# Optimization experiments

Measured on AMD Instinct MI355X. Metric: run time of the kernel, lower is better.

Reference implementation:

```python
import jax, jax.numpy as jnp
import numpy as np

B, N, IN_F, OUT_F, H = 64, 256, 128, 128, 4
NEG_SLOPE = 0.2  # nn.LeakyReLU(dropout) -> slope 0.2


def setup_inputs() -> dict:
    key = jax.random.key(0)
    ks = jax.random.split(key, 10)
    h = jax.random.normal(ks[0], (B, N, IN_F), dtype=jnp.float32)
    projection_matrix = jax.random.normal(ks[1], (B, N, N), dtype=jnp.float32)
    similarity_matrix = jax.random.uniform(ks[2], (B, N, N), dtype=jnp.float32) * 2.0 - 1.0
    quadrant_matrix = jax.random.randint(ks[3], (B, N, N, 2), 0, 4, dtype=jnp.int32)
    # parameters (xavier-ish scaling)
    W = jax.random.normal(ks[4], (IN_F, OUT_F * H), dtype=jnp.float32) / np.sqrt(IN_F)
    a = jax.random.normal(ks[5], (H, 2 * OUT_F, 1), dtype=jnp.float32) / np.sqrt(2 * OUT_F)
    w_proj = jax.random.normal(ks[6], (OUT_F,), dtype=jnp.float32) / np.sqrt(OUT_F)
    w_sim = jax.random.normal(ks[7], (OUT_F,), dtype=jnp.float32) / np.sqrt(OUT_F)
    quadrant_bias = jax.random.normal(ks[8], (4, 4), dtype=jnp.float32) * 0.02
    W_concat = jax.random.normal(ks[9], (OUT_F * H, OUT_F), dtype=jnp.float32) / np.sqrt(OUT_F * H)
    return {"h": h, "projection_matrix": projection_matrix,
            "similarity_matrix": similarity_matrix, "quadrant_matrix": quadrant_matrix,
            "W": W, "a": a, "w_proj": w_proj, "w_sim": w_sim,
            "quadrant_bias": quadrant_bias, "W_concat": W_concat}


def reference(h, projection_matrix, similarity_matrix, quadrant_matrix,
              W, a, w_proj, w_sim, quadrant_bias, W_concat):
    b, n, _ = h.shape
    # Wh_heads: (B, H, N, F)
    Wh = (h @ W).reshape(b, n, H, OUT_F).transpose(0, 2, 1, 3)
    # GAT score: a^T [Wh_i || Wh_j] decomposes into two rank-1 terms
    a1, a2 = a[:, :OUT_F, 0], a[:, OUT_F:, 0]            # (H, F) each
    e_i = jnp.einsum('bhnf,hf->bhn', Wh, a1)
    e_j = jnp.einsum('bhnf,hf->bhn', Wh, a2)
    e = e_i[:, :, :, None] + e_j[:, :, None, :]          # (B, H, N, N)
    e = jnp.where(e > 0, e, NEG_SLOPE * e)               # leaky relu
    # projection bias: <Wh_i, proj[b,i,j] * w_proj> = (Wh_i . w_proj) * proj[b,i,j]
    s_proj = jnp.einsum('bhnf,f->bhn', Wh, w_proj)
    e = e + s_proj[:, :, :, None] * projection_matrix[:, None, :, :]
    # similarity bias, same factored form
    s_sim = jnp.einsum('bhnf,f->bhn', Wh, w_sim)
    e = e + s_sim[:, :, :, None] * similarity_matrix[:, None, :, :]
    # quadrant bias gather
    qb = quadrant_bias[quadrant_matrix[..., 0], quadrant_matrix[..., 1]]  # (B, N, N)
    e = e + qb[:, None, :, :]
    attn = jax.nn.softmax(e, axis=-1)                    # dropout is identity in eval
    h_prime = jnp.einsum('bhij,bhjf->bhif', attn, Wh)    # (B, H, N, F)
    h_prime = h_prime.transpose(0, 2, 1, 3).reshape(b, n, H * OUT_F) @ W_concat
    return jax.nn.elu(h_prime)
```

## Files before the change

### kernel.cpp

```cpp
#include <hip/hip_runtime.h>
#include <math.h>

#define BB 64
#define NN 256
#define IN_F 128
#define OF 128
#define HH 4
#define NEG_SLOPE 0.2f

typedef __attribute__((ext_vector_type(8))) short short8;
typedef __attribute__((ext_vector_type(4))) float f32x4;

#define MFMA16(a, b, c) __builtin_amdgcn_mfma_f32_16x16x32_bf16(a, b, c, 0, 0, 0)

__device__ inline unsigned short f2bf(float x) {
    unsigned u = __float_as_uint(x);
    u += 0x7fff + ((u >> 16) & 1);
    return (unsigned short)(u >> 16);
}

__global__ __launch_bounds__(256) void k0_prep(const int* __restrict__ qm,
        const float* __restrict__ W, const float* __restrict__ Wc,
        unsigned char* __restrict__ qidx, unsigned short* __restrict__ Wt,
        unsigned short* __restrict__ Wct) {
    __shared__ float hl[16][516];
    int blk = blockIdx.x, t = threadIdx.x;
    if (blk < 2048) {
        const int4* qp = (const int4*)qm;
        size_t base = (size_t)blk * 1024;
#pragma unroll
        for (int it = 0; it < 4; it++) {
            size_t i4 = base + it * 256 + t;
            int4 v = qp[i4];
            unsigned short pk = (unsigned short)((v.x * 4 + v.y) | ((v.z * 4 + v.w) << 8));
            ((unsigned short*)qidx)[i4] = pk;
        }
    } else if (blk < 2056) {
        int k0 = (blk - 2048) * 16;
#pragma unroll
        for (int it = 0; it < 8; it++) {
            int li = it * 256 + t;
            int row = li >> 7, col4 = li & 127;
            float4 v = ((const float4*)(W + (size_t)(k0 + row) * 512))[col4];
            *(float4*)&hl[row][col4 * 4] = v;
        }
        __syncthreads();
#pragma unroll
        for (int cc = 0; cc < 2; cc++) {
            int c = t * 2 + cc;
            short8 s0, s1;
#pragma unroll
            for (int k = 0; k < 8; k++) s0[k] = (short)f2bf(hl[k][c]);
#pragma unroll
            for (int k = 0; k < 8; k++) s1[k] = (short)f2bf(hl[k + 8][c]);
            unsigned short* dst = Wt + (size_t)c * 128 + k0;
            *(short8*)dst = s0;
            *(short8*)(dst + 8) = s1;
        }
    } else {
        int k0 = (blk - 2056) * 16;
#pragma unroll
        for (int it = 0; it < 2; it++) {
            int li = it * 256 + t;
            int row = li >> 5, col4 = li & 31;
            float4 v = ((const float4*)(Wc + (size_t)(k0 + row) * 128))[col4];
            *(float4*)&hl[row][col4 * 4] = v;
        }
        __syncthreads();
        if (t < 128) {
            int c = t;
            short8 s0, s1;
#pragma unroll
            for (int k = 0; k < 8; k++) s0[k] = (short)f2bf(hl[k][c]);
#pragma unroll
            for (int k = 0; k < 8; k++) s1[k] = (short)f2bf(hl[k + 8][c]);
            unsigned short* dst = Wct + (size_t)c * 512 + k0;
            *(short8*)dst = s0;
            *(short8*)(dst + 8) = s1;
        }
    }
}

__global__ __launch_bounds__(256) void k1_wh(const float* __restrict__ h,
        const unsigned short* __restrict__ Wt, const float* __restrict__ a,
        const float* __restrict__ w_proj, const float* __restrict__ w_sim,
        unsigned short* __restrict__ Wht, float* __restrict__ ei,
        float* __restrict__ ej, float* __restrict__ sp, float* __restrict__ ss) {
    __shared__ __align__(16) unsigned char hs[8192];
    __shared__ float a1s[512], a2s[512], wps[128], wss[128];
    int l = blockIdx.x;
    int b = l >> 3, n0 = (l & 7) * 32;
    int t = threadIdx.x;
    for (int idx = t; idx < 512; idx += 256) {
        int hh = idx >> 7, f = idx & 127;
        a1s[idx] = a[hh * 256 + f];
        a2s[idx] = a[hh * 256 + 128 + f];
    }
    if (t < 128) { wps[t] = w_proj[t]; wss[t] = w_sim[t]; }
    {
        const float4* hsrc = (const float4*)(h + ((size_t)b * NN + n0) * IN_F);
#pragma unroll
        for (int it = 0; it < 4; it++) {
            int li = it * 256 + t;
            float4 v = hsrc[li];
            int row = li >> 5, col4 = li & 31;
            ushort4 o;
            o.x = f2bf(v.x); o.y = f2bf(v.y); o.z = f2bf(v.z); o.w = f2bf(v.w);
            *(ushort4*)(hs + row * 256 + ((col4 * 8) ^ ((row & 7) << 4))) = o;
        }
    }
    __syncthreads();

    int w = t >> 6, lane = t & 63;
    int cc = lane & 15, g = lane >> 4;

    short8 bh[2][4];
#pragma unroll
    for (int tn = 0; tn < 2; tn++) {
        int row = tn * 16 + cc;
#pragma unroll
        for (int ks = 0; ks < 4; ks++)
            bh[tn][ks] = *(const short8*)(hs + row * 256 + ((ks * 64 + g * 16) ^ ((row & 7) << 4)));
    }

    float q[2][4][4] = {{{0.f}}};
    unsigned short* whb = Wht + (size_t)(b * HH + w) * OF * NN;

#pragma unroll
    for (int tf = 0; tf < 8; tf++) {
        int f = tf * 16 + cc;
        short8 aw[4];
#pragma unroll
        for (int ks = 0; ks < 4; ks++)
            aw[ks] = *(const short8*)(Wt + (size_t)(w * 128 + f) * IN_F + ks * 32 + g * 8);
        f32x4 acc[2];
        acc[0] = (f32x4)(0.f); acc[1] = (f32x4)(0.f);
#pragma unroll
        for (int ks = 0; ks < 4; ks++) {
            acc[0] = MFMA16(bh[0][ks], aw[ks], acc[0]);
            acc[1] = MFMA16(bh[1][ks], aw[ks], acc[1]);
        }
        float c1 = a1s[w * 128 + f], c2 = a2s[w * 128 + f];
        float c3 = wps[f], c4 = wss[f];
#pragma unroll
        for (int tn = 0; tn < 2; tn++) {
            ushort4 o;
            o.x = f2bf(acc[tn][0]); o.y = f2bf(acc[tn][1]);
            o.z = f2bf(acc[tn][2]); o.w = f2bf(acc[tn][3]);
            *(ushort4*)(whb + (size_t)f * NN + n0 + tn * 16 + g * 4) = o;
#pragma unroll
            for (int r = 0; r < 4; r++) {
                float v = acc[tn][r];
                q[tn][0][r] += v * c1; q[tn][1][r] += v * c2;
                q[tn][2][r] += v * c3; q[tn][3][r] += v * c4;
            }
        }
    }
#pragma unroll
    for (int tn = 0; tn < 2; tn++)
#pragma unroll
        for (int ty = 0; ty < 4; ty++)
#pragma unroll
            for (int r = 0; r < 4; r++) {
                float v = q[tn][ty][r];
                v += __shfl_xor(v, 1); v += __shfl_xor(v, 2);
                v += __shfl_xor(v, 4); v += __shfl_xor(v, 8);
                q[tn][ty][r] = v;
            }
    if (cc == 0) {
#pragma unroll
        for (int tn = 0; tn < 2; tn++) {
            size_t base = (size_t)(b * HH + w) * NN + n0 + tn * 16 + g * 4;
            *(float4*)&ei[base] = make_float4(q[tn][0][0], q[tn][0][1], q[tn][0][2], q[tn][0][3]);
            *(float4*)&ej[base] = make_float4(q[tn][1][0], q[tn][1][1], q[tn][1][2], q[tn][1][3]);
            *(float4*)&sp[base] = make_float4(q[tn][2][0], q[tn][2][1], q[tn][2][2], q[tn][2][3]);
            *(float4*)&ss[base] = make_float4(q[tn][3][0], q[tn][3][1], q[tn][3][2], q[tn][3][3]);
        }
    }
}

__global__ __launch_bounds__(256) void k2_fused(
        const float* __restrict__ proj, const float* __restrict__ sim,
        const unsigned char* __restrict__ qidx, const float* __restrict__ qbias,
        const float* __restrict__ ei, const float* __restrict__ ej,
        const float* __restrict__ sp, const float* __restrict__ ss,
        const unsigned short* __restrict__ Wht, const unsigned short* __restrict__ Wct,
        float* __restrict__ out) {
    __shared__ __align__(16) char at_lds[32768];
    __shared__ __align__(16) float ejs[1024];
    __shared__ float eis[HH][16], sps[HH][16], sss[HH][16];
    __shared__ float qb_s[16];

    int l = blockIdx.x;
    int xcd = l & 7, m = l >> 3;
    int b = xcd + ((m >> 4) << 3);
    int i0 = (m & 15) * 16;
    int t = threadIdx.x;
    int wave = t >> 6, lane = t & 63;

    for (int c = t; c < HH * NN; c += 256)
        ejs[c] = ej[(size_t)b * HH * NN + c];
    if (t < 64) {
        int hh = t >> 4, ii = t & 15;
        size_t base = ((size_t)b * HH + hh) * NN + i0 + ii;
        eis[hh][ii] = ei[base]; sps[hh][ii] = sp[base]; sss[hh][ii] = ss[base];
    }
    if (t < 16) qb_s[t] = qbias[t];
    __syncthreads();

    int j0 = lane * 4;
    float4 P4[4], S4[4];
    unsigned qi[4];
#pragma unroll
    for (int rr = 0; rr < 4; rr++) {
        int i = i0 + wave * 4 + rr;
        size_t rb = ((size_t)b * NN + i) * NN + j0;
        P4[rr] = *(const float4*)&proj[rb];
        S4[rr] = *(const float4*)&sim[rb];
        qi[rr] = *(const unsigned*)(qidx + rb);
    }
#pragma unroll
    for (int rr = 0; rr < 4; rr++) {
        int ii = wave * 4 + rr;
        float qb0 = qb_s[qi[rr] & 15];
        float qb1 = qb_s[(qi[rr] >> 8) & 15];
        float qb2 = qb_s[(qi[rr] >> 16) & 15];
        float qb3 = qb_s[(qi[rr] >> 24) & 15];
        float e[HH][4];
#pragma unroll
        for (int hh = 0; hh < HH; hh++) {
            float4 ej4 = *(const float4*)&ejs[hh * 256 + j0];
            float bi = eis[hh][ii], spv = sps[hh][ii], ssv = sss[hh][ii];
            float x;
            x = bi + ej4.x; x = x > 0.f ? x : NEG_SLOPE * x; e[hh][0] = x + spv * P4[rr].x + ssv * S4[rr].x + qb0;
            x = bi + ej4.y; x = x > 0.f ? x : NEG_SLOPE * x; e[hh][1] = x + spv * P4[rr].y + ssv * S4[rr].y + qb1;
            x = bi + ej4.z; x = x > 0.f ? x : NEG_SLOPE * x; e[hh][2] = x + spv * P4[rr].z + ssv * S4[rr].z + qb2;
            x = bi + ej4.w; x = x > 0.f ? x : NEG_SLOPE * x; e[hh][3] = x + spv * P4[rr].w + ssv * S4[rr].w + qb3;
        }
        float mx[HH];
#pragma unroll
        for (int hh = 0; hh < HH; hh++)
            mx[hh] = fmaxf(fmaxf(e[hh][0], e[hh][1]), fmaxf(e[hh][2], e[hh][3]));
#pragma unroll
        for (int off = 32; off; off >>= 1)
#pragma unroll
            for (int hh = 0; hh < HH; hh++)
                mx[hh] = fmaxf(mx[hh], __shfl_xor(mx[hh], off));
        float s[HH];
#pragma unroll
        for (int hh = 0; hh < HH; hh++) {
            e[hh][0] = __expf(e[hh][0] - mx[hh]);
            e[hh][1] = __expf(e[hh][1] - mx[hh]);
            e[hh][2] = __expf(e[hh][2] - mx[hh]);
            e[hh][3] = __expf(e[hh][3] - mx[hh]);
            s[hh] = (e[hh][0] + e[hh][1]) + (e[hh][2] + e[hh][3]);
        }
#pragma unroll
        for (int off = 32; off; off >>= 1)
#pragma unroll
            for (int hh = 0; hh < HH; hh++) s[hh] += __shfl_xor(s[hh], off);
#pragma unroll
        for (int hh = 0; hh < HH; hh++) {
            float inv = 1.0f / s[hh];
            ushort4 pk;
            pk.x = f2bf(e[hh][0] * inv);
            pk.y = f2bf(e[hh][1] * inv);
            pk.z = f2bf(e[hh][2] * inv);
            pk.w = f2bf(e[hh][3] * inv);
            int off2 = hh * 8192 + ii * 512 + ((j0 * 2) ^ ((ii & 7) << 4));
            *(ushort4*)(at_lds + off2) = pk;
        }
    }
    __syncthreads();

    int w = wave;
    int row = lane & 15, g = lane >> 4;
    short8 af[8];
#pragma unroll
    for (int ks = 0; ks < 8; ks++) {
        int off = w * 8192 + row * 512 + ((ks * 64 + g * 16) ^ ((row & 7) << 4));
        af[ks] = *(const short8*)(at_lds + off);
    }
    __syncthreads();

    f32x4 acc[8];
#pragma unroll
    for (int ft = 0; ft < 8; ft++) acc[ft] = (f32x4)(0.f);
    const unsigned short* whb = Wht + (size_t)(b * HH + w) * OF * NN;
#pragma unroll
    for (int ft = 0; ft < 8; ft++) {
        const unsigned short* wb = whb + (size_t)(ft * 16 + row) * NN + g * 8;
#pragma unroll
        for (int ks = 0; ks < 8; ks++) {
            short8 bf = *(const short8*)(wb + ks * 32);
            acc[ft] = MFMA16(af[ks], bf, acc[ft]);
        }
    }
#pragma unroll
    for (int ft = 0; ft < 8; ft++)
#pragma unroll
        for (int r = 0; r < 4; r++) {
            int i = g * 4 + r;
            int kf = w * 128 + ft * 16 + row;
            int off = i * 1024 + ((kf * 2) ^ ((i & 7) << 4));
            *(unsigned short*)(at_lds + off) = f2bf(acc[ft][r]);
        }
    __syncthreads();

    short8 ah[16];
#pragma unroll
    for (int ks = 0; ks < 16; ks++) {
        int off = row * 1024 + ((ks * 64 + g * 16) ^ ((row & 7) << 4));
        ah[ks] = *(const short8*)(at_lds + off);
    }
    f32x4 o2[2];
    o2[0] = (f32x4)(0.f); o2[1] = (f32x4)(0.f);
#pragma unroll
    for (int ct = 0; ct < 2; ct++) {
        int c = (w * 2 + ct) * 16 + row;
        const unsigned short* wc = Wct + (size_t)c * 512 + g * 8;
#pragma unroll
        for (int ks = 0; ks < 16; ks++) {
            short8 bf = *(const short8*)(wc + ks * 32);
            o2[ct] = MFMA16(ah[ks], bf, o2[ct]);
        }
    }
#pragma unroll
    for (int ct = 0; ct < 2; ct++)
#pragma unroll
        for (int r = 0; r < 4; r++) {
            float v = o2[ct][r];
            v = v > 0.f ? v : expm1f(v);
            int i = i0 + g * 4 + r;
            int c = (w * 2 + ct) * 16 + row;
            out[((size_t)b * NN + i) * OF + c] = v;
        }
}

extern "C" void kernel_launch(void* const* d_in, const int* in_sizes, int n_in,
                              void* d_out, int out_size, void* d_ws, size_t ws_size,
                              hipStream_t stream) {
    const float* h      = (const float*)d_in[0];
    const float* proj   = (const float*)d_in[1];
    const float* sim    = (const float*)d_in[2];
    const int*   qm     = (const int*)d_in[3];
    const float* W      = (const float*)d_in[4];
    const float* a      = (const float*)d_in[5];
    const float* w_proj = (const float*)d_in[6];
    const float* w_sim  = (const float*)d_in[7];
    const float* qbias  = (const float*)d_in[8];
    const float* Wc     = (const float*)d_in[9];
    float* out = (float*)d_out;

    unsigned short* Wt  = (unsigned short*)d_ws;
    unsigned short* Wct = Wt + 512 * 128;
    unsigned short* Wht = Wct + 128 * 512;
    float* ei = (float*)(Wht + (size_t)BB * HH * OF * NN);
    float* ej = ei + (size_t)BB * HH * NN;
    float* sp = ej + (size_t)BB * HH * NN;
    float* ss = sp + (size_t)BB * HH * NN;
    unsigned char* qidx = (unsigned char*)(ss + (size_t)BB * HH * NN);

    k0_prep<<<2088, 256, 0, stream>>>(qm, W, Wc, qidx, Wt, Wct);
    k1_wh<<<512, 256, 0, stream>>>(h, Wt, a, w_proj, w_sim, Wht, ei, ej, sp, ss);
    k2_fused<<<BB * 16, 256, 0, stream>>>(proj, sim, qidx, qbias, ei, ej, sp, ss, Wht, Wct, out);
}
```

Measured before the change: 198.5 us.

## Split fused attention kernel and read quadrant matrix directly instead of repacking

Drops the quadrant-index packing pass from the prep kernel, so the attention-score kernel reads the int32 quadrant pairs directly. The old fused kernel is split in two: one computes softmax attention and writes it to global memory as bf16, the other loads that and runs the two MFMA GEMMs. This removes a full separate pass over the quadrant matrix and frees LDS in the GEMM kernel. In exchange it adds an extra kernel launch and a 32 MB bf16 attention round-trip through global memory.

```diff
diff --git a/kernel.cpp b/kernel.cpp
--- a/kernel.cpp
+++ b/kernel.cpp
@@ -19,24 +19,13 @@
     return (unsigned short)(u >> 16);
 }
 
-__global__ __launch_bounds__(256) void k0_prep(const int* __restrict__ qm,
-        const float* __restrict__ W, const float* __restrict__ Wc,
-        unsigned char* __restrict__ qidx, unsigned short* __restrict__ Wt,
+__global__ __launch_bounds__(256) void k0_prep(const float* __restrict__ W,
+        const float* __restrict__ Wc, unsigned short* __restrict__ Wt,
         unsigned short* __restrict__ Wct) {
     __shared__ float hl[16][516];
     int blk = blockIdx.x, t = threadIdx.x;
-    if (blk < 2048) {
-        const int4* qp = (const int4*)qm;
-        size_t base = (size_t)blk * 1024;
-#pragma unroll
-        for (int it = 0; it < 4; it++) {
-            size_t i4 = base + it * 256 + t;
-            int4 v = qp[i4];
-            unsigned short pk = (unsigned short)((v.x * 4 + v.y) | ((v.z * 4 + v.w) << 8));
-            ((unsigned short*)qidx)[i4] = pk;
-        }
-    } else if (blk < 2056) {
-        int k0 = (blk - 2048) * 16;
+    if (blk < 8) {
+        int k0 = blk * 16;
 #pragma unroll
         for (int it = 0; it < 8; it++) {
             int li = it * 256 + t;
@@ -58,7 +47,7 @@
             *(short8*)(dst + 8) = s1;
         }
     } else {
-        int k0 = (blk - 2056) * 16;
+        int k0 = (blk - 8) * 16;
 #pragma unroll
         for (int it = 0; it < 2; it++) {
             int li = it * 256 + t;
@@ -179,22 +168,18 @@
     }
 }
 
-__global__ __launch_bounds__(256) void k2_fused(
+__global__ __launch_bounds__(256) void kb_attn(
         const float* __restrict__ proj, const float* __restrict__ sim,
-        const unsigned char* __restrict__ qidx, const float* __restrict__ qbias,
+        const int* __restrict__ qm, const float* __restrict__ qbias,
         const float* __restrict__ ei, const float* __restrict__ ej,
         const float* __restrict__ sp, const float* __restrict__ ss,
-        const unsigned short* __restrict__ Wht, const unsigned short* __restrict__ Wct,
-        float* __restrict__ out) {
-    __shared__ __align__(16) char at_lds[32768];
+        unsigned short* __restrict__ attn_g) {
     __shared__ __align__(16) float ejs[1024];
     __shared__ float eis[HH][16], sps[HH][16], sss[HH][16];
     __shared__ float qb_s[16];
-
     int l = blockIdx.x;
-    int xcd = l & 7, m = l >> 3;
-    int b = xcd + ((m >> 4) << 3);
-    int i0 = (m & 15) * 16;
+    int b = l >> 4;
+    int i0 = (l & 15) * 16;
     int t = threadIdx.x;
     int wave = t >> 6, lane = t & 63;
 
@@ -209,33 +194,26 @@
     __syncthreads();
 
     int j0 = lane * 4;
-    float4 P4[4], S4[4];
-    unsigned qi[4];
-#pragma unroll
-    for (int rr = 0; rr < 4; rr++) {
-        int i = i0 + wave * 4 + rr;
-        size_t rb = ((size_t)b * NN + i) * NN + j0;
-        P4[rr] = *(const float4*)&proj[rb];
-        S4[rr] = *(const float4*)&sim[rb];
-        qi[rr] = *(const unsigned*)(qidx + rb);
-    }
-#pragma unroll
     for (int rr = 0; rr < 4; rr++) {
         int ii = wave * 4 + rr;
-        float qb0 = qb_s[qi[rr] & 15];
-        float qb1 = qb_s[(qi[rr] >> 8) & 15];
-        float qb2 = qb_s[(qi[rr] >> 16) & 15];
-        float qb3 = qb_s[(qi[rr] >> 24) & 15];
+        int i = i0 + ii;
+        size_t rb = ((size_t)b * NN + i) * NN + j0;
+        float4 P4 = *(const float4*)&proj[rb];
+        float4 S4 = *(const float4*)&sim[rb];
+        int4 qa = *(const int4*)&qm[rb * 2];
+        int4 qc = *(const int4*)&qm[rb * 2 + 4];
+        float qb0 = qb_s[qa.x * 4 + qa.y], qb1 = qb_s[qa.z * 4 + qa.w];
+        float qb2 = qb_s[qc.x * 4 + qc.y], qb3 = qb_s[qc.z * 4 + qc.w];
         float e[HH][4];
 #pragma unroll
         for (int hh = 0; hh < HH; hh++) {
             float4 ej4 = *(const float4*)&ejs[hh * 256 + j0];
             float bi = eis[hh][ii], spv = sps[hh][ii], ssv = sss[hh][ii];
             float x;
-            x = bi + ej4.x; x = x > 0.f ? x : NEG_SLOPE * x; e[hh][0] = x + spv * P4[rr].x + ssv * S4[rr].x + qb0;
-            x = bi + ej4.y; x = x > 0.f ? x : NEG_SLOPE * x; e[hh][1] = x + spv * P4[rr].y + ssv * S4[rr].y + qb1;
-            x = bi + ej4.z; x = x > 0.f ? x : NEG_SLOPE * x; e[hh][2] = x + spv * P4[rr].z + ssv * S4[rr].z + qb2;
-            x = bi + ej4.w; x = x > 0.f ? x : NEG_SLOPE * x; e[hh][3] = x + spv * P4[rr].w + ssv * S4[rr].w + qb3;
+            x = bi + ej4.x; x = x > 0.f ? x : NEG_SLOPE * x; e[hh][0] = x + spv * P4.x + ssv * S4.x + qb0;
+            x = bi + ej4.y; x = x > 0.f ? x : NEG_SLOPE * x; e[hh][1] = x + spv * P4.y + ssv * S4.y + qb1;
+            x = bi + ej4.z; x = x > 0.f ? x : NEG_SLOPE * x; e[hh][2] = x + spv * P4.z + ssv * S4.z + qb2;
+            x = bi + ej4.w; x = x > 0.f ? x : NEG_SLOPE * x; e[hh][3] = x + spv * P4.w + ssv * S4.w + qb3;
         }
         float mx[HH];
 #pragma unroll
@@ -267,21 +245,29 @@
             pk.y = f2bf(e[hh][1] * inv);
             pk.z = f2bf(e[hh][2] * inv);
             pk.w = f2bf(e[hh][3] * inv);
-            int off2 = hh * 8192 + ii * 512 + ((j0 * 2) ^ ((ii & 7) << 4));
-            *(ushort4*)(at_lds + off2) = pk;
-        }
-    }
-    __syncthreads();
-
-    int w = wave;
+            *(ushort4*)(attn_g + (((size_t)b * HH + hh) * NN + i) * NN + j0) = pk;
+        }
+    }
+}
+
+__global__ __launch_bounds__(256) void kc_pv(
+        const unsigned short* __restrict__ attn_g,
+        const unsigned short* __restrict__ Wht, const unsigned short* __restrict__ Wct,
+        float* __restrict__ out) {
+    __shared__ __align__(16) char hp_lds[16384];
+    int l = blockIdx.x;
+    int xcd = l & 7, m = l >> 3;
+    int b = xcd + ((m >> 4) << 3);
+    int i0 = (m & 15) * 16;
+    int t = threadIdx.x;
+    int w = t >> 6, lane = t & 63;
     int row = lane & 15, g = lane >> 4;
+
+    const unsigned short* ab = attn_g + (((size_t)b * HH + w) * NN + i0 + row) * NN + g * 8;
     short8 af[8];
 #pragma unroll
-    for (int ks = 0; ks < 8; ks++) {
-        int off = w * 8192 + row * 512 + ((ks * 64 + g * 16) ^ ((row & 7) << 4));
-        af[ks] = *(const short8*)(at_lds + off);
-    }
-    __syncthreads();
+    for (int ks = 0; ks < 8; ks++)
+        af[ks] = *(const short8*)(ab + ks * 32);
 
     f32x4 acc[8];
 #pragma unroll
@@ -303,7 +289,7 @@
             int i = g * 4 + r;
             int kf = w * 128 + ft * 16 + row;
             int off = i * 1024 + ((kf * 2) ^ ((i & 7) << 4));
-            *(unsigned short*)(at_lds + off) = f2bf(acc[ft][r]);
+            *(unsigned short*)(hp_lds + off) = f2bf(acc[ft][r]);
         }
     __syncthreads();
 
@@ -311,7 +297,7 @@
 #pragma unroll
     for (int ks = 0; ks < 16; ks++) {
         int off = row * 1024 + ((ks * 64 + g * 16) ^ ((row & 7) << 4));
-        ah[ks] = *(const short8*)(at_lds + off);
+        ah[ks] = *(const short8*)(hp_lds + off);
     }
     f32x4 o2[2];
     o2[0] = (f32x4)(0.f); o2[1] = (f32x4)(0.f);
@@ -359,9 +345,10 @@
     float* ej = ei + (size_t)BB * HH * NN;
     float* sp = ej + (size_t)BB * HH * NN;
     float* ss = sp + (size_t)BB * HH * NN;
-    unsigned char* qidx = (unsigned char*)(ss + (size_t)BB * HH * NN);
-
-    k0_prep<<<2088, 256, 0, stream>>>(qm, W, Wc, qidx, Wt, Wct);
+    unsigned short* attn_g = (unsigned short*)(ss + (size_t)BB * HH * NN);
+
+    k0_prep<<<40, 256, 0, stream>>>(W, Wc, Wt, Wct);
     k1_wh<<<512, 256, 0, stream>>>(h, Wt, a, w_proj, w_sim, Wht, ei, ej, sp, ss);
-    k2_fused<<<BB * 16, 256, 0, stream>>>(proj, sim, qidx, qbias, ei, ej, sp, ss, Wht, Wct, out);
-}
+    kb_attn<<<BB * 16, 256, 0, stream>>>(proj, sim, qm, qbias, ei, ej, sp, ss, attn_g);
+    kc_pv<<<BB * 16, 256, 0, stream>>>(attn_g, Wht, Wct, out);
+}
```

Result: faster. 190.4 us (-4.1%).
